# Kernel optimization log

Hardware: AMD Instinct MI355X
Metric: run time of the kernel (lower is better)

## Reference

```python
import jax, jax.numpy as jnp
import numpy as np


def _entmax15(x, axis=-1):
    # Faithful port of Entmax15Function (alpha=1.5 entmax, closed-form via sort).
    x = x - jnp.max(x, axis=axis, keepdims=True)  # numerical stability
    x = x / 2.0                                   # alpha=1.5 rescaling
    d = x.shape[axis]
    # sort descending along axis
    xsrt = -jnp.sort(-x, axis=axis)
    shape = [1] * x.ndim
    shape[axis] = d
    rho = jnp.arange(1, d + 1, dtype=x.dtype).reshape(shape)
    mean = jnp.cumsum(xsrt, axis=axis) / rho
    mean_sq = jnp.cumsum(xsrt * xsrt, axis=axis) / rho
    ss = rho * (mean_sq - mean * mean)
    delta = (1.0 - ss) / rho
    delta_nz = jnp.maximum(delta, 0.0)
    tau = mean - jnp.sqrt(delta_nz)
    # support size: number of sorted entries with tau <= xsrt
    support_size = jnp.sum((tau <= xsrt).astype(jnp.int32), axis=axis, keepdims=True)
    tau_star = jnp.take_along_axis(tau, support_size - 1, axis=axis)
    y = jnp.maximum(x - tau_star, 0.0)
    return y * y


def setup_inputs() -> dict:
    key = jax.random.key(0)
    x = jax.random.normal(key, (4096, 32000), dtype=jnp.float32)
    return {"x": x}


def reference(x) -> jnp.ndarray:
    return _entmax15(x, axis=-1)
```

## Files before the change

### kernel.cpp

```cpp
#include <hip/hip_runtime.h>
#include <math.h>


#define ROWLEN 32000
#define ROWV4  8000
#define BLOCK  1024
#define NV4    8
#define NW     16
#define CAND_MAX 4096
#define GRID   256

typedef float f32x4 __attribute__((ext_vector_type(4)));

__device__ __forceinline__ void wg_barrier() {
  asm volatile("s_waitcnt lgkmcnt(0)" ::: "memory");
  __builtin_amdgcn_sched_barrier(0);
  __builtin_amdgcn_s_barrier();
  __builtin_amdgcn_sched_barrier(0);
}

__device__ __forceinline__ void wait_own_row() {
  asm volatile("s_waitcnt vmcnt(8)" ::: "memory");
  __builtin_amdgcn_sched_barrier(0);
}

__device__ __forceinline__ void issue_row(f32x4 (&v)[NV4],
                                          const float* __restrict__ rowp,
                                          int t) {
#pragma unroll
  for (int i = 0; i < NV4; ++i) {
    int idx = i * BLOCK + t;
    idx = idx < ROWV4 ? idx : 0;
    const float* p = rowp + (size_t)idx * 4;
    asm volatile("global_load_dwordx4 %0, %1, off"
                 : "=&v"(v[i]) : "v"(p) : "memory");
  }
}

__global__ __launch_bounds__(BLOCK)
void entmax15_kernel(const float* __restrict__ x, float* __restrict__ out,
                     int rows, int rpb) {
  const int t    = threadIdx.x;
  const int lane = t & 63;
  const int wid  = t >> 6;

  __shared__ float s_max[NW];
  __shared__ int   s_total;
  __shared__ float s_tau;
  __shared__ float s_cand[CAND_MAX];

  const int rbeg = blockIdx.x * rpb;
  const int rend = min(rbeg + rpb, rows);
  if (rbeg >= rend) return;

  f32x4 A[NV4], B[NV4];

  auto process = [&](f32x4 (&v)[NV4], int row) {
    if (t == 0) s_total = 0;

    float lmax = -1e30f;
#pragma unroll
    for (int i = 0; i < NV4; ++i) {
      int idx = i * BLOCK + t;
      if (idx < ROWV4)
        lmax = fmaxf(lmax,
                     fmaxf(fmaxf(v[i].x, v[i].y), fmaxf(v[i].z, v[i].w)));
    }
#pragma unroll
    for (int m = 32; m >= 1; m >>= 1) lmax = fmaxf(lmax, __shfl_xor(lmax, m));
    if (lane == 0) s_max[wid] = lmax;
    wg_barrier();
    float xmax = s_max[0];
#pragma unroll
    for (int w = 1; w < NW; ++w) xmax = fmaxf(xmax, s_max[w]);
    const float thr = xmax - 2.0f;

    int c = 0;
#pragma unroll
    for (int i = 0; i < NV4; ++i) {
      int idx = i * BLOCK + t;
      if (idx < ROWV4)
        c += (v[i].x > thr) + (v[i].y > thr) + (v[i].z > thr) + (v[i].w > thr);
    }
    int incl = c;
#pragma unroll
    for (int m = 1; m < 64; m <<= 1) {
      int nb = __shfl_up(incl, m);
      if (lane >= m) incl += nb;
    }
    int wbase = 0;
    if (lane == 63) wbase = atomicAdd(&s_total, incl);
    wbase = __shfl(wbase, 63);
    {
      int off = wbase + incl - c;
#pragma unroll
      for (int i = 0; i < NV4; ++i) {
        int idx = i * BLOCK + t;
        if (idx < ROWV4) {
          float a;
          a = v[i].x; if (a > thr) { if (off < CAND_MAX) s_cand[off] = (a - xmax) * 0.5f; ++off; }
          a = v[i].y; if (a > thr) { if (off < CAND_MAX) s_cand[off] = (a - xmax) * 0.5f; ++off; }
          a = v[i].z; if (a > thr) { if (off < CAND_MAX) s_cand[off] = (a - xmax) * 0.5f; ++off; }
          a = v[i].w; if (a > thr) { if (off < CAND_MAX) s_cand[off] = (a - xmax) * 0.5f; ++off; }
        }
      }
    }
    wg_barrier();
    const int total = min(s_total, CAND_MAX);

    if (wid == 0) {
      float tau = -1.0f;
      const int ng = (total + 511) >> 9;
      for (int it = 0; it < 6; ++it) {
        float s = 0.f, q = 0.f;
        for (int g = 0; g < ng; ++g) {
#pragma unroll
          for (int k = 0; k < 8; ++k) {
            int j = lane + ((g << 3) + k) * 64;
            float z = s_cand[j & (CAND_MAX - 1)];
            float d = z - tau;
            if (j < total && d > 0.f) { s += d; q += d * d; }
          }
        }
#pragma unroll
        for (int m = 32; m >= 1; m >>= 1) {
          s += __shfl_xor(s, m);
          q += __shfl_xor(q, m);
        }
        if (s > 0.f) tau += (q - 1.0f) / (2.0f * s);
      }
      for (int it = 0; it < 2; ++it) {
        float kk = 0.f, s1 = 0.f, s2 = 0.f;
        for (int g = 0; g < ng; ++g) {
#pragma unroll
          for (int k = 0; k < 8; ++k) {
            int j = lane + ((g << 3) + k) * 64;
            float z = s_cand[j & (CAND_MAX - 1)];
            if (j < total && z > tau) { kk += 1.f; s1 += z; s2 += z * z; }
          }
        }
#pragma unroll
        for (int m = 32; m >= 1; m >>= 1) {
          kk += __shfl_xor(kk, m);
          s1 += __shfl_xor(s1, m);
          s2 += __shfl_xor(s2, m);
        }
        float disc = s1 * s1 - kk * (s2 - 1.0f);
        tau = (s1 - sqrtf(fmaxf(disc, 0.f))) / kk;
      }
      if (lane == 0) s_tau = tau;
    }
    wg_barrier();
    const float cc = fmaf(xmax, 0.5f, s_tau);

    f32x4* __restrict__ outr = (f32x4*)(out + (size_t)row * ROWLEN);
#pragma unroll
    for (int i = 0; i < NV4; ++i) {
      int idx = i * BLOCK + t;
      if (idx < ROWV4) {
        f32x4 o;
        float d;
        d = fmaf(v[i].x, 0.5f, -cc); o.x = d > 0.f ? d * d : 0.f;
        d = fmaf(v[i].y, 0.5f, -cc); o.y = d > 0.f ? d * d : 0.f;
        d = fmaf(v[i].z, 0.5f, -cc); o.z = d > 0.f ? d * d : 0.f;
        d = fmaf(v[i].w, 0.5f, -cc); o.w = d > 0.f ? d * d : 0.f;
        __builtin_nontemporal_store(o, &outr[idx]);
      }
    }
  };

  issue_row(A, x + (size_t)rbeg * ROWLEN, t);
  {
    int rB0 = (rbeg + 1 < rend) ? rbeg + 1 : rbeg;
    issue_row(B, x + (size_t)rB0 * ROWLEN, t);
  }
  for (int r = rbeg; r < rend; r += 2) {
    wait_own_row();
    process(A, r);
    if (r + 2 < rend) issue_row(A, x + (size_t)(r + 2) * ROWLEN, t);
    if (r + 1 >= rend) break;
    wait_own_row();
    process(B, r + 1);
    if (r + 3 < rend) issue_row(B, x + (size_t)(r + 3) * ROWLEN, t);
  }
}

extern "C" void kernel_launch(void* const* d_in, const int* in_sizes, int n_in,
                              void* d_out, int out_size, void* d_ws, size_t ws_size,
                              hipStream_t stream) {
  const float* x = (const float*)d_in[0];
  float* out = (float*)d_out;
  int rows = in_sizes[0] / ROWLEN;
  int grid = rows < GRID ? rows : GRID;
  int rpb  = (rows + grid - 1) / grid;
  hipLaunchKernelGGL(entmax15_kernel, dim3(grid), dim3(BLOCK), 0, stream,
                     x, out, rows, rpb);
}
```

Before: 247.4 us.

## Stage input rows through LDS with direct global-to-LDS loads

Replaces the two-register-buffer row prefetch with global_load_lds DMA into a 128KB LDS row buffer. Each wave now owns a contiguous 500-vector chunk of the row. The next row is staged right after the current one is copied into registers, and a vmcnt wait at the end of the iteration covers it. Output stores become plain stores instead of nontemporal, and the candidate buffer shrinks to 2048. This is meant to cut VGPR pressure and register-load latency, but it leaves only one row in flight and uses a large share of LDS.

```diff
diff --git a/kernel.cpp b/kernel.cpp
--- a/kernel.cpp
+++ b/kernel.cpp
@@ -1,16 +1,19 @@
 #include <hip/hip_runtime.h>
 #include <math.h>
+#include <stdint.h>
 
 
 #define ROWLEN 32000
-#define ROWV4  8000
 #define BLOCK  1024
-#define NV4    8
 #define NW     16
-#define CAND_MAX 4096
+#define CHUNK  500
+#define NB     8
+#define CAND_MAX 2048
 #define GRID   256
 
 typedef float f32x4 __attribute__((ext_vector_type(4)));
+typedef __attribute__((address_space(1))) const void gvoid;
+typedef __attribute__((address_space(3))) void lvoid;
 
 __device__ __forceinline__ void wg_barrier() {
   asm volatile("s_waitcnt lgkmcnt(0)" ::: "memory");
@@ -18,23 +21,17 @@
   __builtin_amdgcn_s_barrier();
   __builtin_amdgcn_sched_barrier(0);
 }
-
-__device__ __forceinline__ void wait_own_row() {
+__device__ __forceinline__ void wait_vm0() {
+  asm volatile("s_waitcnt vmcnt(0)" ::: "memory");
+  __builtin_amdgcn_sched_barrier(0);
+}
+__device__ __forceinline__ void wait_vm8() {
   asm volatile("s_waitcnt vmcnt(8)" ::: "memory");
   __builtin_amdgcn_sched_barrier(0);
 }
-
-__device__ __forceinline__ void issue_row(f32x4 (&v)[NV4],
-                                          const float* __restrict__ rowp,
-                                          int t) {
-#pragma unroll
-  for (int i = 0; i < NV4; ++i) {
-    int idx = i * BLOCK + t;
-    idx = idx < ROWV4 ? idx : 0;
-    const float* p = rowp + (size_t)idx * 4;
-    asm volatile("global_load_dwordx4 %0, %1, off"
-                 : "=&v"(v[i]) : "v"(p) : "memory");
-  }
+__device__ __forceinline__ void wait_lgkm0() {
+  asm volatile("s_waitcnt lgkmcnt(0)" ::: "memory");
+  __builtin_amdgcn_sched_barrier(0);
 }
 
 __global__ __launch_bounds__(BLOCK)
@@ -44,6 +41,7 @@
   const int lane = t & 63;
   const int wid  = t >> 6;
 
+  __shared__ f32x4 s_row[NW * NB * 64];
   __shared__ float s_max[NW];
   __shared__ int   s_total;
   __shared__ float s_tau;
@@ -53,18 +51,29 @@
   const int rend = min(rbeg + rpb, rows);
   if (rbeg >= rend) return;
 
-  f32x4 A[NV4], B[NV4];
-
-  auto process = [&](f32x4 (&v)[NV4], int row) {
+  auto stage = [&](int row) {
+    const float* rowp = x + (size_t)row * ROWLEN;
+#pragma unroll
+    for (int i = 0; i < NB; ++i) {
+      int l = i * 64 + lane;
+      int e = wid * CHUNK + (l < CHUNK ? l : 0);
+      const float* g = rowp + (size_t)e * 4;
+      f32x4* d = &s_row[(wid * NB + i) * 64];
+      __builtin_amdgcn_global_load_lds((gvoid*)g, (lvoid*)d, 16, 0, 0);
+    }
+  };
+
+  stage(rbeg);
+  wait_vm0();
+
+  for (int r = rbeg; r < rend; ++r) {
     if (t == 0) s_total = 0;
 
     float lmax = -1e30f;
 #pragma unroll
-    for (int i = 0; i < NV4; ++i) {
-      int idx = i * BLOCK + t;
-      if (idx < ROWV4)
-        lmax = fmaxf(lmax,
-                     fmaxf(fmaxf(v[i].x, v[i].y), fmaxf(v[i].z, v[i].w)));
+    for (int i = 0; i < NB; ++i) {
+      f32x4 u = s_row[(wid * NB + i) * 64 + lane];
+      lmax = fmaxf(lmax, fmaxf(fmaxf(u.x, u.y), fmaxf(u.z, u.w)));
     }
 #pragma unroll
     for (int m = 32; m >= 1; m >>= 1) lmax = fmaxf(lmax, __shfl_xor(lmax, m));
@@ -75,18 +84,25 @@
     for (int w = 1; w < NW; ++w) xmax = fmaxf(xmax, s_max[w]);
     const float thr = xmax - 2.0f;
 
+    f32x4 v[NB];
+#pragma unroll
+    for (int i = 0; i < NB; ++i) v[i] = s_row[(wid * NB + i) * 64 + lane];
+    wait_lgkm0();
+
+    stage(r + 1 < rend ? r + 1 : rend - 1);
+
     int c = 0;
 #pragma unroll
-    for (int i = 0; i < NV4; ++i) {
-      int idx = i * BLOCK + t;
-      if (idx < ROWV4)
+    for (int i = 0; i < NB; ++i) {
+      int l = i * 64 + lane;
+      if (l < CHUNK)
         c += (v[i].x > thr) + (v[i].y > thr) + (v[i].z > thr) + (v[i].w > thr);
     }
     int incl = c;
 #pragma unroll
     for (int m = 1; m < 64; m <<= 1) {
-      int nb = __shfl_up(incl, m);
-      if (lane >= m) incl += nb;
+      int nb2 = __shfl_up(incl, m);
+      if (lane >= m) incl += nb2;
     }
     int wbase = 0;
     if (lane == 63) wbase = atomicAdd(&s_total, incl);
@@ -94,9 +110,9 @@
     {
       int off = wbase + incl - c;
 #pragma unroll
-      for (int i = 0; i < NV4; ++i) {
-        int idx = i * BLOCK + t;
-        if (idx < ROWV4) {
+      for (int i = 0; i < NB; ++i) {
+        int l = i * 64 + lane;
+        if (l < CHUNK) {
           float a;
           a = v[i].x; if (a > thr) { if (off < CAND_MAX) s_cand[off] = (a - xmax) * 0.5f; ++off; }
           a = v[i].y; if (a > thr) { if (off < CAND_MAX) s_cand[off] = (a - xmax) * 0.5f; ++off; }
@@ -153,35 +169,21 @@
     wg_barrier();
     const float cc = fmaf(xmax, 0.5f, s_tau);
 
-    f32x4* __restrict__ outr = (f32x4*)(out + (size_t)row * ROWLEN);
-#pragma unroll
-    for (int i = 0; i < NV4; ++i) {
-      int idx = i * BLOCK + t;
-      if (idx < ROWV4) {
-        f32x4 o;
-        float d;
-        d = fmaf(v[i].x, 0.5f, -cc); o.x = d > 0.f ? d * d : 0.f;
-        d = fmaf(v[i].y, 0.5f, -cc); o.y = d > 0.f ? d * d : 0.f;
-        d = fmaf(v[i].z, 0.5f, -cc); o.z = d > 0.f ? d * d : 0.f;
-        d = fmaf(v[i].w, 0.5f, -cc); o.w = d > 0.f ? d * d : 0.f;
-        __builtin_nontemporal_store(o, &outr[idx]);
-      }
-    }
-  };
-
-  issue_row(A, x + (size_t)rbeg * ROWLEN, t);
-  {
-    int rB0 = (rbeg + 1 < rend) ? rbeg + 1 : rbeg;
-    issue_row(B, x + (size_t)rB0 * ROWLEN, t);
-  }
-  for (int r = rbeg; r < rend; r += 2) {
-    wait_own_row();
-    process(A, r);
-    if (r + 2 < rend) issue_row(A, x + (size_t)(r + 2) * ROWLEN, t);
-    if (r + 1 >= rend) break;
-    wait_own_row();
-    process(B, r + 1);
-    if (r + 3 < rend) issue_row(B, x + (size_t)(r + 3) * ROWLEN, t);
+    f32x4* __restrict__ outv = (f32x4*)(out + (size_t)r * ROWLEN);
+#pragma unroll
+    for (int i = 0; i < NB; ++i) {
+      int l = i * 64 + lane;
+      int e = wid * CHUNK + (l < CHUNK ? l : 0);
+      f32x4 o;
+      float d;
+      d = fmaf(v[i].x, 0.5f, -cc); o.x = d > 0.f ? d * d : 0.f;
+      d = fmaf(v[i].y, 0.5f, -cc); o.y = d > 0.f ? d * d : 0.f;
+      d = fmaf(v[i].z, 0.5f, -cc); o.z = d > 0.f ? d * d : 0.f;
+      d = fmaf(v[i].w, 0.5f, -cc); o.w = d > 0.f ? d * d : 0.f;
+      outv[e] = o;
+    }
+
+    wait_vm8();
   }
 }
 
```

Result: no change. 251.9 us (+1.8%).
